# Optimization experiments

Hardware: AMD Instinct MI355X
Metric: run time of the kernel (lower is better)

The kernel has to match this reference:

```python
import jax, jax.numpy as jnp
import numpy as np

B, S, D, H = 2, 2048, 1024, 16
HD = D // H  # head_dim = 64


def setup_inputs() -> dict:
    key = jax.random.key(0)
    ks = jax.random.split(key, 6)
    sc = 0.02
    return {
        "x": jax.random.normal(ks[0], (B, S, D), dtype=jnp.float32),
        "W_query": jax.random.normal(ks[1], (D, D), dtype=jnp.float32) * sc,
        "W_key": jax.random.normal(ks[2], (D, D), dtype=jnp.float32) * sc,
        "W_value": jax.random.normal(ks[3], (D, D), dtype=jnp.float32) * sc,
        "W_out": jax.random.normal(ks[4], (D, D), dtype=jnp.float32) * sc,
        "b_out": jnp.zeros((D,), dtype=jnp.float32),
    }


def reference(x, W_query, W_key, W_value, W_out, b_out):
    b, s, _ = x.shape
    # torch nn.Linear: y = x @ W.T ; split into heads [b, h, s, hd]
    def proj(W):
        return (x @ W.T).reshape(b, s, H, HD).transpose(0, 2, 1, 3)

    q, k, v = proj(W_query), proj(W_key), proj(W_value)
    scores = jnp.einsum("bhqd,bhkd->bhqk", q, k)  # [b, h, s, s]
    causal = jnp.tril(jnp.ones((s, s), dtype=bool))  # True = keep
    scores = jnp.where(causal, scores, -jnp.inf)
    weights = jax.nn.softmax(scores / np.sqrt(HD).astype(np.float32), axis=-1)
    # dropout p=0.0 -> identity
    ctx = jnp.einsum("bhqk,bhkd->bhqd", weights, v)
    ctx = ctx.transpose(0, 2, 1, 3).reshape(b, s, D)
    return ctx @ W_out.T + b_out
```

## Files before the change

kernel.cpp:

```cpp
#include <hip/hip_runtime.h>
#include <stdint.h>

#define B_  2
#define S_  2048
#define D_  1024
#define H_  16
#define HD_ 64
#define M_  (B_*S_)

typedef __attribute__((ext_vector_type(8)))  short bf16x8;
typedef __attribute__((ext_vector_type(4)))  float f32x4;
typedef __attribute__((ext_vector_type(16))) float f32x16;
typedef __attribute__((ext_vector_type(4)))  unsigned int u32x4;


__device__ __forceinline__ unsigned short f2bf(float f) {
    unsigned int u = __float_as_uint(f);
    unsigned int r = (u + 0x7fffu + ((u >> 16) & 1u)) >> 16;
    return (unsigned short)r;
}

__device__ __forceinline__ unsigned int cvt_pk_bf16(float lo, float hi) {
    unsigned int r;
    asm("v_cvt_pk_bf16_f32 %0, %1, %2" : "=v"(r) : "v"(lo), "v"(hi));
    return r;
}

__device__ __forceinline__ float fexp2(float x) {
    float r;
    asm("v_exp_f32 %0, %1" : "=v"(r) : "v"(x));
    return r;
}

__device__ __forceinline__ void gload_lds16(const void* g, void* l) {
    __builtin_amdgcn_global_load_lds(
        (const __attribute__((address_space(1))) unsigned int*)g,
        (__attribute__((address_space(3))) unsigned int*)l,
        16, 0, 0);
}


__global__ __launch_bounds__(256) void cast_all(
    const float* __restrict__ x,
    const float* __restrict__ wq, const float* __restrict__ wk,
    const float* __restrict__ wv, const float* __restrict__ wo,
    unsigned short* __restrict__ dst)
{
    int b = blockIdx.x;
    const float* src;
    size_t soff, doff;
    float sc = 1.0f;
    if (b < 2048) {
        src = x; soff = (size_t)b * 2048; doff = soff;
    } else {
        int r  = (b - 2048) >> 9;
        int lb = (b - 2048) & 511;
        src = (r == 0) ? wq : (r == 1) ? wk : (r == 2) ? wv : wo;
        if (r <= 1) sc = 0.4246609093670877f;
        soff = (size_t)lb * 2048;
        doff = (size_t)4194304 + (size_t)r * 1048576 + soff;
    }
    int idx = threadIdx.x * 8;
    float4 a = *reinterpret_cast<const float4*>(src + soff + idx);
    float4 c = *reinterpret_cast<const float4*>(src + soff + idx + 4);
    unsigned short t[8];
    t[0]=f2bf(a.x*sc); t[1]=f2bf(a.y*sc); t[2]=f2bf(a.z*sc); t[3]=f2bf(a.w*sc);
    t[4]=f2bf(c.x*sc); t[5]=f2bf(c.y*sc); t[6]=f2bf(c.z*sc); t[7]=f2bf(c.w*sc);
    *reinterpret_cast<uint4*>(dst + doff + idx) = *reinterpret_cast<const uint4*>(t);
}


__global__ __launch_bounds__(256) void gemm_qkv(
    const unsigned short* __restrict__ A,
    const unsigned short* __restrict__ Bm,
    unsigned short* __restrict__ Cqk,
    unsigned short* __restrict__ Vt)
{
    constexpr int BK = 64, K = 1024;
    __shared__ unsigned short As[128 * BK];
    __shared__ unsigned short Bs[128 * BK];

    const int tid  = threadIdx.x;
    const int lane = tid & 63;
    const int wid  = tid >> 6;
    const int wr = wid >> 1, wc = wid & 1;
    const int l31 = lane & 31, hi = lane >> 5;

    const int lin  = blockIdx.x;
    const int wgid = (lin & 7) * 96 + (lin >> 3);
    const int tm = (wgid / 24) * 128, tn = (wgid % 24) * 128;

    f32x16 acc[2][2] = {};

    const int srow8 = lane >> 3;
    const int scol  = ((lane & 7) ^ srow8) * 8;

    for (int k0 = 0; k0 < K; k0 += BK) {
        __syncthreads();
        #pragma unroll
        for (int i = 0; i < 4; ++i) {
            int row = i * 32 + wid * 8 + srow8;
            gload_lds16(A  + (size_t)(tm + row) * K + k0 + scol,
                        (void*)(As + i * 2048 + wid * 512));
            gload_lds16(Bm + (size_t)(tn + row) * K + k0 + scol,
                        (void*)(Bs + i * 2048 + wid * 512));
        }
        __syncthreads();

        #pragma unroll
        for (int ks = 0; ks < 4; ++ks) {
            bf16x8 af[2], bfr[2];
            #pragma unroll
            for (int ar = 0; ar < 2; ++ar) {
                int r = wr * 64 + ar * 32 + l31;
                af[ar] = *reinterpret_cast<const bf16x8*>(
                    As + r * BK + (((ks * 2 + hi) ^ (r & 7)) * 8));
            }
            #pragma unroll
            for (int br = 0; br < 2; ++br) {
                int r = wc * 64 + br * 32 + l31;
                bfr[br] = *reinterpret_cast<const bf16x8*>(
                    Bs + r * BK + (((ks * 2 + hi) ^ (r & 7)) * 8));
            }
            #pragma unroll
            for (int ar = 0; ar < 2; ++ar)
                #pragma unroll
                for (int br = 0; br < 2; ++br)
                    acc[ar][br] = __builtin_amdgcn_mfma_f32_32x32x16_bf16(
                        af[ar], bfr[br], acc[ar][br], 0, 0, 0);
        }
    }

    const bool isV = (tn >= 2048);
    #pragma unroll
    for (int ar = 0; ar < 2; ++ar) {
        #pragma unroll
        for (int br = 0; br < 2; ++br) {
            int col = tn + wc * 64 + br * 32 + l31;
            if (!isV) {
                #pragma unroll
                for (int g = 0; g < 4; ++g)
                    #pragma unroll
                    for (int r4 = 0; r4 < 4; ++r4) {
                        int row = tm + wr * 64 + ar * 32 + g * 8 + 4 * hi + r4;
                        Cqk[(size_t)row * 2048 + col] = f2bf(acc[ar][br][g * 4 + r4]);
                    }
            } else {
                #pragma unroll
                for (int g = 0; g < 4; ++g) {
                    unsigned short t[4];
                    #pragma unroll
                    for (int r4 = 0; r4 < 4; ++r4) t[r4] = f2bf(acc[ar][br][g * 4 + r4]);
                    int row0 = tm + wr * 64 + ar * 32 + g * 8 + 4 * hi;
                    *reinterpret_cast<uint2*>(Vt + (size_t)(col - 2048) * M_ + row0) =
                        *reinterpret_cast<const uint2*>(t);
                }
            }
        }
    }
}


__global__ __launch_bounds__(256) void gemm_out(
    const unsigned short* __restrict__ A,
    const unsigned short* __restrict__ Bm,
    float* __restrict__ C,
    const float* __restrict__ bias)
{
    constexpr int BK = 64, K = 1024, N = 1024;
    __shared__ unsigned short As[128 * BK];
    __shared__ unsigned short Bs[64 * BK];

    const int tid  = threadIdx.x;
    const int lane = tid & 63;
    const int wid  = tid >> 6;
    const int wr = wid >> 1, wc = wid & 1;
    const int l31 = lane & 31, hi = lane >> 5;

    const int lin  = blockIdx.x;
    const int wgid = (lin & 7) * 64 + (lin >> 3);
    const int tm = (wgid >> 4) * 128, tn = (wgid & 15) * 64;

    f32x16 acc[2] = {};

    const int srow8 = lane >> 3;
    const int scol  = ((lane & 7) ^ srow8) * 8;

    for (int k0 = 0; k0 < K; k0 += BK) {
        __syncthreads();
        #pragma unroll
        for (int i = 0; i < 4; ++i) {
            int row = i * 32 + wid * 8 + srow8;
            gload_lds16(A + (size_t)(tm + row) * K + k0 + scol,
                        (void*)(As + i * 2048 + wid * 512));
        }
        #pragma unroll
        for (int i = 0; i < 2; ++i) {
            int row = i * 32 + wid * 8 + srow8;
            gload_lds16(Bm + (size_t)(tn + row) * K + k0 + scol,
                        (void*)(Bs + i * 2048 + wid * 512));
        }
        __syncthreads();

        #pragma unroll
        for (int ks = 0; ks < 4; ++ks) {
            bf16x8 af[2], bfr;
            #pragma unroll
            for (int ar = 0; ar < 2; ++ar) {
                int r = wr * 64 + ar * 32 + l31;
                af[ar] = *reinterpret_cast<const bf16x8*>(
                    As + r * BK + (((ks * 2 + hi) ^ (r & 7)) * 8));
            }
            {
                int r = wc * 32 + l31;
                bfr = *reinterpret_cast<const bf16x8*>(
                    Bs + r * BK + (((ks * 2 + hi) ^ (r & 7)) * 8));
            }
            #pragma unroll
            for (int ar = 0; ar < 2; ++ar)
                acc[ar] = __builtin_amdgcn_mfma_f32_32x32x16_bf16(
                    af[ar], bfr, acc[ar], 0, 0, 0);
        }
    }

    {
        int col = tn + wc * 32 + l31;
        float bv = bias[col];
        #pragma unroll
        for (int ar = 0; ar < 2; ++ar)
            #pragma unroll
            for (int g = 0; g < 4; ++g)
                #pragma unroll
                for (int r4 = 0; r4 < 4; ++r4) {
                    int row = tm + wr * 64 + ar * 32 + g * 8 + 4 * hi + r4;
                    C[(size_t)row * N + col] = acc[ar][g * 4 + r4] + bv;
                }
    }
}


__global__ __launch_bounds__(256, 4) void attn_kernel(
    const unsigned short* __restrict__ QK,
    const unsigned short* __restrict__ VT,
    unsigned short* __restrict__ Ctx)
{
    __shared__ unsigned short Ks[4][32 * 64];
    __shared__ unsigned short Vs[4][64 * 32];

    const int tid  = threadIdx.x;
    const int lane = tid & 63;
    const int wid  = tid >> 6;
    const int l31  = lane & 31;
    const int hi   = lane >> 5;

    const int lin  = blockIdx.x;
    const int idx  = lin >> 3;
    const int bh   = (lin & 7) + 8 * (idx & 3);
    const int qb   = 63 - (idx >> 2);
    const int b = bh >> 4, h = bh & 15;
    const size_t baseRow = (size_t)b * S_;
    const int qw = qb * 32;
    const int q  = qw + l31;

    bf16x8 qf[4];
    #pragma unroll
    for (int s = 0; s < 4; ++s)
        qf[s] = *reinterpret_cast<const bf16x8*>(
            QK + (baseRow + q) * 2048 + h * HD_ + s * 16 + hi * 8);

    float l = 0.0f;
    f32x16 oacc[2] = {};

    const int nkt = qb + 1;

    const int kr  = lane >> 3;
    const int ks  = lane & 7;
    const int vr  = lane >> 2;
    const int vsl = lane & 3;

#define STAGE_K(kt_) do {                                                      \
    int k0_ = (kt_) * 32;                                                      \
    _Pragma("unroll")                                                          \
    for (int i_ = 0; i_ < 4; ++i_) {                                           \
        int krow_ = i_ * 8 + kr;                                               \
        int ksc_  = (ks ^ kr) * 8;                                             \
        gload_lds16(QK + (baseRow + k0_ + krow_) * 2048 + D_ + h * HD_ + ksc_, \
                    (void*)(&Ks[wid][i_ * 512]));                              \
    } } while (0)
#define STAGE_V(kt_) do {                                                      \
    int k0_ = (kt_) * 32;                                                      \
    _Pragma("unroll")                                                          \
    for (int i_ = 0; i_ < 4; ++i_) {                                           \
        int vrow_ = i_ * 16 + vr;                                              \
        int vsc_  = (vsl ^ ((vrow_ >> 1) & 3)) * 8;                            \
        gload_lds16(VT + (size_t)(h * HD_ + vrow_) * M_ + baseRow + k0_ + vsc_,\
                    (void*)(&Vs[wid][i_ * 512]));                              \
    } } while (0)

    if (wid < nkt) {
        STAGE_K(wid);
        STAGE_V(wid);
        for (int kt = wid; kt < nkt; kt += 4) {
            const bool more = (kt + 4 < nkt);

            asm volatile("s_waitcnt vmcnt(4)" ::: "memory");

            const unsigned short* Kc = &Ks[wid][0];

            f32x16 sc = {};
            #pragma unroll
            for (int s = 0; s < 4; ++s) {
                int sl = (2 * s + hi) ^ (l31 & 7);
                bf16x8 kf = *reinterpret_cast<const bf16x8*>(Kc + l31 * 64 + sl * 8);
                sc = __builtin_amdgcn_mfma_f32_32x32x16_bf16(kf, qf[s], sc, 0, 0, 0);
            }

            asm volatile("s_waitcnt lgkmcnt(0)" ::: "memory");
            __builtin_amdgcn_sched_barrier(0);
            if (more) STAGE_K(kt + 4);

            if (kt == qb) {
                #pragma unroll
                for (int r = 0; r < 16; ++r) {
                    int kl = kt * 32 + (r & 3) + 8 * (r >> 2) + 4 * hi;
                    if (kl > q) sc[r] = -INFINITY;
                }
            }

            unsigned int g0, g1, g2, g3, g4, g5, g6, g7;
            float ps = 0.0f;
            {
                float e0, e1, e2, e3;
                e0=fexp2(sc[0]);  e1=fexp2(sc[1]);  e2=fexp2(sc[2]);  e3=fexp2(sc[3]);
                ps += (e0+e1)+(e2+e3); g0 = cvt_pk_bf16(e0,e1); g1 = cvt_pk_bf16(e2,e3);
                e0=fexp2(sc[4]);  e1=fexp2(sc[5]);  e2=fexp2(sc[6]);  e3=fexp2(sc[7]);
                ps += (e0+e1)+(e2+e3); g2 = cvt_pk_bf16(e0,e1); g3 = cvt_pk_bf16(e2,e3);
                e0=fexp2(sc[8]);  e1=fexp2(sc[9]);  e2=fexp2(sc[10]); e3=fexp2(sc[11]);
                ps += (e0+e1)+(e2+e3); g4 = cvt_pk_bf16(e0,e1); g5 = cvt_pk_bf16(e2,e3);
                e0=fexp2(sc[12]); e1=fexp2(sc[13]); e2=fexp2(sc[14]); e3=fexp2(sc[15]);
                ps += (e0+e1)+(e2+e3); g6 = cvt_pk_bf16(e0,e1); g7 = cvt_pk_bf16(e2,e3);
            }
            l += ps;

            asm("v_permlane32_swap_b32 %0, %1" : "+v"(g0), "+v"(g2));
            asm("v_permlane32_swap_b32 %0, %1" : "+v"(g1), "+v"(g3));
            asm("v_permlane32_swap_b32 %0, %1" : "+v"(g4), "+v"(g6));
            asm("v_permlane32_swap_b32 %0, %1" : "+v"(g5), "+v"(g7));
            bf16x8 pa0 = __builtin_bit_cast(bf16x8, (u32x4){g0, g1, g2, g3});
            bf16x8 pa1 = __builtin_bit_cast(bf16x8, (u32x4){g4, g5, g6, g7});

            if (more) asm volatile("s_waitcnt vmcnt(4)" ::: "memory");
            else      asm volatile("s_waitcnt vmcnt(0)" ::: "memory");

            const unsigned short* Vc = &Vs[wid][0];
            bf16x8 vf[2][2];
            #pragma unroll
            for (int dt = 0; dt < 2; ++dt)
                #pragma unroll
                for (int s = 0; s < 2; ++s) {
                    int d = dt * 32 + l31;
                    int sl = (2 * s + hi) ^ ((d >> 1) & 3);
                    vf[dt][s] = *reinterpret_cast<const bf16x8*>(Vc + d * 32 + sl * 8);
                }

            asm volatile("s_waitcnt lgkmcnt(0)" ::: "memory");
            __builtin_amdgcn_sched_barrier(0);
            if (more) STAGE_V(kt + 4);

            __builtin_amdgcn_s_setprio(1);
            #pragma unroll
            for (int dt = 0; dt < 2; ++dt) {
                oacc[dt] = __builtin_amdgcn_mfma_f32_32x32x16_bf16(pa0, vf[dt][0], oacc[dt], 0, 0, 0);
                oacc[dt] = __builtin_amdgcn_mfma_f32_32x32x16_bf16(pa1, vf[dt][1], oacc[dt], 0, 0, 0);
            }
            __builtin_amdgcn_s_setprio(0);
        }
    }
#undef STAGE_K
#undef STAGE_V

    float* Olw = (float*)&Ks[wid][0];
    float* Lpw = (float*)&Vs[wid][0];
    float lc = l + __shfl_xor(l, 32, 64);
    if (hi == 0) Lpw[l31] = lc;

    const int cq = tid >> 3;
    const int cd = (tid & 7) * 4;
    float inv = 0.0f;
    #pragma unroll
    for (int ph = 0; ph < 2; ++ph) {
        __syncthreads();
        #pragma unroll
        for (int r = 0; r < 16; ++r) {
            int qr = (r & 3) + 8 * (r >> 2) + 4 * hi;
            Olw[qr * 32 + l31] = oacc[ph][r];
        }
        __syncthreads();
        float s0 = 0, s1 = 0, s2 = 0, s3 = 0, lt = 0;
        #pragma unroll
        for (int w = 0; w < 4; ++w) {
            const float* O = (const float*)&Ks[w][0];
            f32x4 a = *reinterpret_cast<const f32x4*>(O + cq * 32 + cd);
            s0 += a[0]; s1 += a[1]; s2 += a[2]; s3 += a[3];
            if (ph == 0) lt += ((const float*)&Vs[w][0])[cq];
        }
        if (ph == 0) inv = 1.0f / lt;
        unsigned short o[4];
        o[0] = f2bf(s0 * inv); o[1] = f2bf(s1 * inv);
        o[2] = f2bf(s2 * inv); o[3] = f2bf(s3 * inv);
        *reinterpret_cast<uint2*>(
            Ctx + (baseRow + qw + cq) * D_ + h * HD_ + ph * 32 + cd) =
            *reinterpret_cast<const uint2*>(o);
    }
}


extern "C" void kernel_launch(void* const* d_in, const int* in_sizes, int n_in,
                              void* d_out, int out_size, void* d_ws, size_t ws_size,
                              hipStream_t stream) {
    const float* x  = (const float*)d_in[0];
    const float* wq = (const float*)d_in[1];
    const float* wk = (const float*)d_in[2];
    const float* wv = (const float*)d_in[3];
    const float* wo = (const float*)d_in[4];
    const float* bo = (const float*)d_in[5];

    unsigned short* ws = (unsigned short*)d_ws;
    unsigned short* xb  = ws;
    unsigned short* wqb = xb  + 4194304;
    unsigned short* wob = wqb + 3145728;
    unsigned short* QKb = wob + 1048576;
    unsigned short* VT  = QKb + 8388608;
    unsigned short* Cx  = VT  + 4194304;

    cast_all<<<4096, 256, 0, stream>>>(x, wq, wk, wv, wo, xb);

    gemm_qkv<<<768, 256, 0, stream>>>(xb, wqb, QKb, VT);

    attn_kernel<<<2048, 256, 0, stream>>>(QKb, VT, Cx);

    gemm_out<<<512, 256, 0, stream>>>(Cx, wob, (float*)d_out, bo);
}
```

Baseline: 96.71 us.

## Double-buffer QKV GEMM LDS loads and shrink M tile to 64

The QKV projection GEMM now prefetches the next K-slice into a second LDS buffer while computing on the current one, replacing the two-barrier load/compute loop with a single barrier per step. The M tile drops from 128 to 64 rows, doubling the grid to 1536 workgroups, and the block-ID swizzle is changed to match. The aim is to hide global-load latency and improve CU fill, at the cost of halving per-wave MFMA work per A fragment, which lowers operand reuse and raises B-tile traffic.

```diff
diff --git a/kernel.cpp b/kernel.cpp
--- a/kernel.cpp
+++ b/kernel.cpp
@@ -76,9 +76,9 @@
     unsigned short* __restrict__ Cqk,
     unsigned short* __restrict__ Vt)
 {
-    constexpr int BK = 64, K = 1024;
-    __shared__ unsigned short As[128 * BK];
-    __shared__ unsigned short Bs[128 * BK];
+    constexpr int BK = 64, K = 1024, NT = K / BK;
+    __shared__ unsigned short As[2][64 * BK];
+    __shared__ unsigned short Bs[2][128 * BK];
 
     const int tid  = threadIdx.x;
     const int lane = tid & 63;
@@ -87,74 +87,79 @@
     const int l31 = lane & 31, hi = lane >> 5;
 
     const int lin  = blockIdx.x;
-    const int wgid = (lin & 7) * 96 + (lin >> 3);
-    const int tm = (wgid / 24) * 128, tn = (wgid % 24) * 128;
-
-    f32x16 acc[2][2] = {};
-
-    const int srow8 = lane >> 3;
-    const int scol  = ((lane & 7) ^ srow8) * 8;
-
-    for (int k0 = 0; k0 < K; k0 += BK) {
-        __syncthreads();
-        #pragma unroll
-        for (int i = 0; i < 4; ++i) {
-            int row = i * 32 + wid * 8 + srow8;
-            gload_lds16(A  + (size_t)(tm + row) * K + k0 + scol,
-                        (void*)(As + i * 2048 + wid * 512));
-            gload_lds16(Bm + (size_t)(tn + row) * K + k0 + scol,
-                        (void*)(Bs + i * 2048 + wid * 512));
-        }
-        __syncthreads();
-
+    const int wgid = (lin & 7) * 192 + (lin >> 3);
+    const int tn = (wgid >> 6) * 128;
+    const int tm = (wgid & 63) * 64;
+
+    f32x16 acc[2] = {};
+
+    const int sr8 = wid * 8 + (lane >> 3);
+    const int ssl = lane & 7;
+
+#define QSTAGE(t_, bi_) do {                                                   \
+    int k0_ = (t_) * BK;                                                       \
+    _Pragma("unroll")                                                          \
+    for (int i_ = 0; i_ < 2; ++i_) {                                           \
+        int row_ = i_ * 32 + sr8;                                              \
+        int sc_ = (ssl ^ (row_ & 7)) * 8;                                      \
+        gload_lds16(A + (size_t)(tm + row_) * K + k0_ + sc_,                   \
+                    (void*)(&As[bi_][i_ * 2048 + wid * 512]));                 \
+    }                                                                          \
+    _Pragma("unroll")                                                          \
+    for (int i_ = 0; i_ < 4; ++i_) {                                           \
+        int row_ = i_ * 32 + sr8;                                              \
+        int sc_ = (ssl ^ (row_ & 7)) * 8;                                      \
+        gload_lds16(Bm + (size_t)(tn + row_) * K + k0_ + sc_,                  \
+                    (void*)(&Bs[bi_][i_ * 2048 + wid * 512]));                 \
+    } } while (0)
+
+    QSTAGE(0, 0);
+
+    for (int t = 0; t < NT; ++t) {
+        asm volatile("s_waitcnt vmcnt(0)" ::: "memory");
+        __builtin_amdgcn_s_barrier();
+        __builtin_amdgcn_sched_barrier(0);
+        if (t + 1 < NT) QSTAGE(t + 1, (t + 1) & 1);
+
+        const unsigned short* Ac = &As[t & 1][0];
+        const unsigned short* Bc = &Bs[t & 1][0];
         #pragma unroll
         for (int ks = 0; ks < 4; ++ks) {
-            bf16x8 af[2], bfr[2];
-            #pragma unroll
-            for (int ar = 0; ar < 2; ++ar) {
-                int r = wr * 64 + ar * 32 + l31;
-                af[ar] = *reinterpret_cast<const bf16x8*>(
-                    As + r * BK + (((ks * 2 + hi) ^ (r & 7)) * 8));
-            }
+            int ra = wr * 32 + l31;
+            bf16x8 af = *reinterpret_cast<const bf16x8*>(
+                Ac + ra * BK + (((ks * 2 + hi) ^ (ra & 7)) * 8));
             #pragma unroll
             for (int br = 0; br < 2; ++br) {
-                int r = wc * 64 + br * 32 + l31;
-                bfr[br] = *reinterpret_cast<const bf16x8*>(
-                    Bs + r * BK + (((ks * 2 + hi) ^ (r & 7)) * 8));
-            }
-            #pragma unroll
-            for (int ar = 0; ar < 2; ++ar)
-                #pragma unroll
-                for (int br = 0; br < 2; ++br)
-                    acc[ar][br] = __builtin_amdgcn_mfma_f32_32x32x16_bf16(
-                        af[ar], bfr[br], acc[ar][br], 0, 0, 0);
-        }
-    }
+                int rb = wc * 64 + br * 32 + l31;
+                bf16x8 bf = *reinterpret_cast<const bf16x8*>(
+                    Bc + rb * BK + (((ks * 2 + hi) ^ (rb & 7)) * 8));
+                acc[br] = __builtin_amdgcn_mfma_f32_32x32x16_bf16(af, bf, acc[br], 0, 0, 0);
+            }
+        }
+    }
+#undef QSTAGE
 
     const bool isV = (tn >= 2048);
     #pragma unroll
-    for (int ar = 0; ar < 2; ++ar) {
-        #pragma unroll
-        for (int br = 0; br < 2; ++br) {
-            int col = tn + wc * 64 + br * 32 + l31;
-            if (!isV) {
+    for (int br = 0; br < 2; ++br) {
+        int col = tn + wc * 64 + br * 32 + l31;
+        if (!isV) {
+            #pragma unroll
+            for (int g = 0; g < 4; ++g)
                 #pragma unroll
-                for (int g = 0; g < 4; ++g)
-                    #pragma unroll
-                    for (int r4 = 0; r4 < 4; ++r4) {
-                        int row = tm + wr * 64 + ar * 32 + g * 8 + 4 * hi + r4;
-                        Cqk[(size_t)row * 2048 + col] = f2bf(acc[ar][br][g * 4 + r4]);
-                    }
-            } else {
+                for (int r4 = 0; r4 < 4; ++r4) {
+                    int row = tm + wr * 32 + g * 8 + 4 * hi + r4;
+                    Cqk[(size_t)row * 2048 + col] = f2bf(acc[br][g * 4 + r4]);
+                }
+        } else {
+            #pragma unroll
+            for (int g = 0; g < 4; ++g) {
+                unsigned short tt[4];
                 #pragma unroll
-                for (int g = 0; g < 4; ++g) {
-                    unsigned short t[4];
-                    #pragma unroll
-                    for (int r4 = 0; r4 < 4; ++r4) t[r4] = f2bf(acc[ar][br][g * 4 + r4]);
-                    int row0 = tm + wr * 64 + ar * 32 + g * 8 + 4 * hi;
-                    *reinterpret_cast<uint2*>(Vt + (size_t)(col - 2048) * M_ + row0) =
-                        *reinterpret_cast<const uint2*>(t);
-                }
+                for (int r4 = 0; r4 < 4; ++r4) tt[r4] = f2bf(acc[br][g * 4 + r4]);
+                int row0 = tm + wr * 32 + g * 8 + 4 * hi;
+                *reinterpret_cast<uint2*>(Vt + (size_t)(col - 2048) * M_ + row0) =
+                    *reinterpret_cast<const uint2*>(tt);
             }
         }
     }
@@ -435,7 +440,7 @@
 
     cast_all<<<4096, 256, 0, stream>>>(x, wq, wk, wv, wo, xb);
 
-    gemm_qkv<<<768, 256, 0, stream>>>(xb, wqb, QKb, VT);
+    gemm_qkv<<<1536, 256, 0, stream>>>(xb, wqb, QKb, VT);
 
     attn_kernel<<<2048, 256, 0, stream>>>(QKb, VT, Cx);
 
```

Measured after the change: 107.8 us. 1.12x slower.
